# Kernel optimization log

Hardware: AMD Instinct MI355X
Metric: run time of the kernel (lower is better)

Reference implementation:

```python
import jax, jax.numpy as jnp
import numpy as np

N_NODES = 50000
N_EDGES = 800000
N_GRAPHS = 1024
BN_EPS = 1e-5

def _linear_params(key, fan_in, fan_out):
    k1, k2 = jax.random.split(key)
    lim = 1.0 / np.sqrt(fan_in)
    w = jax.random.uniform(k1, (fan_in, fan_out), jnp.float32, -lim, lim)
    b = jax.random.uniform(k2, (fan_out,), jnp.float32, -lim, lim)
    return w, b


def setup_inputs() -> dict:
    key = jax.random.key(0)
    ks = jax.random.split(key, 16)
    x = jax.random.normal(ks[0], (N_NODES, 114), jnp.float32)
    edge_index = jax.random.randint(ks[1], (2, N_EDGES), 0, N_NODES, jnp.int64)
    batch = jnp.sort(jax.random.randint(ks[2], (N_NODES,), 0, N_GRAPHS, jnp.int64))
    w1a, b1a = _linear_params(ks[3], 114, 198)
    w1b, b1b = _linear_params(ks[4], 198, 198)
    w2a, b2a = _linear_params(ks[5], 198, 64)
    w2b, b2b = _linear_params(ks[6], 64, 64)
    w3a, b3a = _linear_params(ks[7], 64, 32)
    w3b, b3b = _linear_params(ks[8], 32, 32)
    fw1, fb1 = _linear_params(ks[9], 32, 16)
    fw2, fb2 = _linear_params(ks[10], 16, 8)
    ow, ob = _linear_params(ks[11], 8, 2)
    g1 = jnp.ones((198,), jnp.float32); be1 = jnp.zeros((198,), jnp.float32)
    g2 = jnp.ones((64,), jnp.float32); be2 = jnp.zeros((64,), jnp.float32)
    g3 = jnp.ones((32,), jnp.float32); be3 = jnp.zeros((32,), jnp.float32)
    return dict(x=x, edge_index=edge_index, batch=batch,
                w1a=w1a, b1a=b1a, w1b=w1b, b1b=b1b, g1=g1, be1=be1,
                w2a=w2a, b2a=b2a, w2b=w2b, b2b=b2b, g2=g2, be2=be2,
                w3a=w3a, b3a=b3a, w3b=w3b, b3b=b3b, g3=g3, be3=be3,
                fw1=fw1, fb1=fb1, fw2=fw2, fb2=fb2, ow=ow, ob=ob)


def _gin_conv(x, src, dst, wa, ba, wb, bb):
    # GINConv, eps=0: h_i = MLP((1+eps)*x_i + sum_{j->i} x_j)
    agg = jax.ops.segment_sum(x[src], dst, num_segments=N_NODES)
    h = x + agg
    h = jax.nn.relu(h @ wa + ba) @ wb + bb
    return h


def _batchnorm(h, gamma, beta):
    # training-mode BN over the node axis (biased variance, as torch)
    mean = jnp.mean(h, axis=0)
    var = jnp.var(h, axis=0)
    return (h - mean) * jax.lax.rsqrt(var + BN_EPS) * gamma + beta


def reference(x, edge_index, batch,
              w1a, b1a, w1b, b1b, g1, be1,
              w2a, b2a, w2b, b2b, g2, be2,
              w3a, b3a, w3b, b3b, g3, be3,
              fw1, fb1, fw2, fb2, ow, ob):
    src, dst = edge_index[0], edge_index[1]
    h = jax.nn.relu(_gin_conv(x, src, dst, w1a, b1a, w1b, b1b))
    h = _batchnorm(h, g1, be1)
    h = jax.nn.relu(_gin_conv(h, src, dst, w2a, b2a, w2b, b2b))
    h = _batchnorm(h, g2, be2)
    h = jax.nn.relu(_gin_conv(h, src, dst, w3a, b3a, w3b, b3b))
    h = _batchnorm(h, g3, be3)
    g = jax.ops.segment_sum(h, batch, num_segments=N_GRAPHS)  # global_add_pool
    g = jax.nn.relu(g @ fw1 + fb1)
    g = jax.nn.relu(g @ fw2 + fb2)
    return g @ ow + ob
```

## Files before the change

kernel.cpp:

```cpp
#include <hip/hip_runtime.h>

#define NODES  50000
#define EDGES  800000
#define GRAPHS 1024
#define P      200

#define SCAN_BLK 256
#define SCAN_NB  ((NODES + SCAN_BLK - 1) / SCAN_BLK)

typedef __attribute__((ext_vector_type(8))) short short8v;
typedef __attribute__((ext_vector_type(4))) float f32x4;

__device__ __forceinline__ ushort f2bf(float f) {
    uint u = __float_as_uint(f);
    u = u + 0x7FFFu + ((u >> 16) & 1u);
    return (ushort)(u >> 16);
}

__global__ void hist_kernel(const int* __restrict__ dst, int* __restrict__ deg) {
    int e = blockIdx.x * blockDim.x + threadIdx.x;
    if (e < EDGES) atomicAdd(&deg[dst[e]], 1);
}

__global__ void scan_part(const int* __restrict__ deg, int* __restrict__ part) {
    __shared__ int sh[SCAN_BLK];
    int t = threadIdx.x;
    int n = blockIdx.x * SCAN_BLK + t;
    sh[t] = (n < NODES) ? deg[n] : 0;
    __syncthreads();
    for (int off = SCAN_BLK / 2; off > 0; off >>= 1) {
        if (t < off) sh[t] += sh[t + off];
        __syncthreads();
    }
    if (t == 0) part[blockIdx.x] = sh[0];
}

__global__ void scan_scan(int* __restrict__ part) {
    __shared__ int sh[SCAN_BLK];
    int t = threadIdx.x;
    int v = (t < SCAN_NB) ? part[t] : 0;
    sh[t] = v;
    __syncthreads();
    for (int off = 1; off < SCAN_BLK; off <<= 1) {
        int u = 0;
        if (t >= off) u = sh[t - off];
        __syncthreads();
        if (t >= off) sh[t] += u;
        __syncthreads();
    }
    if (t < SCAN_NB) part[t] = sh[t] - v;
}

__global__ void scan_expand(const int* __restrict__ deg, const int* __restrict__ part,
                            int* __restrict__ rowstart, int* __restrict__ cursor) {
    __shared__ int sh[SCAN_BLK];
    int t = threadIdx.x;
    int n = blockIdx.x * SCAN_BLK + t;
    int v = (n < NODES) ? deg[n] : 0;
    sh[t] = v;
    __syncthreads();
    for (int off = 1; off < SCAN_BLK; off <<= 1) {
        int u = 0;
        if (t >= off) u = sh[t - off];
        __syncthreads();
        if (t >= off) sh[t] += u;
        __syncthreads();
    }
    int excl = sh[t] - v + part[blockIdx.x];
    if (n < NODES) {
        rowstart[n] = excl;
        cursor[n]   = excl;
        if (n == NODES - 1) rowstart[NODES] = excl + v;
    }
}

__global__ void scatter_kernel(const int* __restrict__ src, const int* __restrict__ dst,
                               int* __restrict__ cursor, int* __restrict__ csrc) {
    int e = blockIdx.x * blockDim.x + threadIdx.x;
    if (e < EDGES) {
        int p = atomicAdd(&cursor[dst[e]], 1);
        csrc[p] = src[e];
    }
}

__global__ void pad_w_mfma(const float* __restrict__ W, int K, int N, int NCH, int CT,
                           ushort* __restrict__ out) {
    int s = blockIdx.x * blockDim.x + threadIdx.x;
    int half = NCH * CT * 512;
    if (s >= 2 * half) return;
    int h = s / half;
    int r = s % half;
    int j = r & 7, col = (r >> 3) & 15, kg = (r >> 7) & 3;
    int rest = r >> 9;
    int ct = rest % CT, c = rest / CT;
    int k = c * 32 + kg * 8 + j;
    int n = ct * 16 + col;
    float v = (k < K && n < N) ? W[k * N + n] : 0.0f;
    ushort hi = f2bf(v);
    if (h == 0) out[s] = hi;
    else {
        float hf = __uint_as_float(((uint)hi) << 16);
        out[s] = f2bf(v - hf);
    }
}

template<int D>
__global__ void csr_agg(const float* __restrict__ feat, int fpitch,
                        const int* __restrict__ rowstart, const int* __restrict__ csrc,
                        float* __restrict__ agg, int opitch) {
    int wid  = (blockIdx.x * blockDim.x + threadIdx.x) >> 6;
    int lane = threadIdx.x & 63;
    if (wid >= NODES) return;
    constexpr int NI  = (D + 63) / 64;
    constexpr int UNR = (NI == 1) ? 8 : 4;
    float s[NI];
#pragma unroll
    for (int i = 0; i < NI; i++) s[i] = 0.0f;
    const int r0 = rowstart[wid], r1 = rowstart[wid + 1];
    for (int base = r0; base < r1; base += 64) {
        const int myidx = (base + lane < r1) ? csrc[base + lane] : 0;
        const int cnt = min(64, r1 - base);
        int t = 0;
        for (; t + UNR <= cnt; t += UNR) {
            const float* p[UNR];
#pragma unroll
            for (int u = 0; u < UNR; u++)
                p[u] = feat + (size_t)__shfl(myidx, t + u) * fpitch;
            float v[UNR][NI];
#pragma unroll
            for (int u = 0; u < UNR; u++)
#pragma unroll
                for (int i = 0; i < NI; i++) {
                    int c = lane + 64 * i;
                    if (c < D) v[u][i] = p[u][c];
                }
#pragma unroll
            for (int i = 0; i < NI; i++) {
                int c = lane + 64 * i;
                if (c < D) {
                    float acc = 0.0f;
#pragma unroll
                    for (int u = 0; u < UNR; u++) acc += v[u][i];
                    s[i] += acc;
                }
            }
        }
        for (; t < cnt; t++) {
            const float* fp2 = feat + (size_t)__shfl(myidx, t) * fpitch;
#pragma unroll
            for (int i = 0; i < NI; i++) {
                int c = lane + 64 * i;
                if (c < D) s[i] += fp2[c];
            }
        }
    }
    float* ap = agg + (size_t)wid * opitch;
#pragma unroll
    for (int i = 0; i < NI; i++) {
        int c = lane + 64 * i;
        if (c < D) ap[c] = s[i];
    }
}

template<int K, int N, bool ADD2, bool STATS, bool BNX, bool PRE, bool ACT>
__launch_bounds__(256)
__global__ void gemm_mfma(const float* __restrict__ X, int xpitch,
                          const float* __restrict__ A2, int apitch,
                          const ushort* __restrict__ WF,
                          const float* __restrict__ B,
                          const float* __restrict__ PREB,
                          const float* __restrict__ scale, const float* __restrict__ shift,
                          float* __restrict__ OUT, int opitch,
                          float* __restrict__ gsum, float* __restrict__ gsq) {
    constexpr int KP  = ((K + 31) / 32) * 32;
    constexpr int NCH = KP / 32;
    constexpr int NP  = ((N + 63) / 64) * 64;
    constexpr int CT  = NP / 16;
    constexpr int CTW = CT / 4;
    static_assert(CT % 4 == 0, "col tiles must split across 4 waves");

    __shared__ __align__(16) ushort A_lds[2][4][4][16][8];
    __shared__ float shSum[STATS ? NP : 4];
    __shared__ float shSq [STATS ? NP : 4];

    const int tid  = threadIdx.x;
    const int lane = tid & 63;
    const int wv   = tid >> 6;
    const int node0 = blockIdx.x * 64;

    if (STATS) {
        for (int n = tid; n < NP; n += 256) { shSum[n] = 0.0f; shSq[n] = 0.0f; }
    }

    f32x4 acc[4][CTW] = {};

    const int sr  = tid >> 2;
    const int skg = tid & 3;
    const size_t fstride = (size_t)NCH * CT * 512;

    for (int c = 0; c < NCH; c++) {
        const int kbase = c * 32;
        {
            const int gn = node0 + sr;
            const int k0 = kbase + skg * 8;
            float v[8];
#pragma unroll
            for (int j = 0; j < 8; j++) {
                int gk = k0 + j;
                float t = 0.0f;
                if (gn < NODES && gk < K) {
                    t = X[(size_t)gn * xpitch + gk];
                    if (BNX) t = fmaf(t, scale[gk], shift[gk]);
                    if (ADD2) t += A2[(size_t)gn * apitch + gk];
                    if (PRE)  t = fmaxf(t + PREB[gk], 0.0f);
                }
                v[j] = t;
            }
            short8v hv, lv;
#pragma unroll
            for (int j = 0; j < 8; j++) {
                ushort h = f2bf(v[j]);
                float hf = __uint_as_float(((uint)h) << 16);
                ushort l = f2bf(v[j] - hf);
                hv[j] = (short)h; lv[j] = (short)l;
            }
            *(short8v*)&A_lds[0][sr >> 4][skg][sr & 15][0] = hv;
            *(short8v*)&A_lds[1][sr >> 4][skg][sr & 15][0] = lv;
        }
        __syncthreads();

        const int kg = lane >> 4, rw = lane & 15;
        short8v ah[4], al[4];
#pragma unroll
        for (int rt = 0; rt < 4; rt++) {
            ah[rt] = *(const short8v*)&A_lds[0][rt][kg][rw][0];
            al[rt] = *(const short8v*)&A_lds[1][rt][kg][rw][0];
        }
#pragma unroll
        for (int t = 0; t < CTW; t++) {
            const int ct = wv * CTW + t;
            const size_t fb = ((size_t)(c * CT + ct)) * 512 + (size_t)lane * 8;
            short8v wh = *(const short8v*)(WF + fb);
            short8v wl = *(const short8v*)(WF + fstride + fb);
#pragma unroll
            for (int rt = 0; rt < 4; rt++) {
                acc[rt][t] = __builtin_amdgcn_mfma_f32_16x16x32_bf16(ah[rt], wh, acc[rt][t], 0, 0, 0);
                acc[rt][t] = __builtin_amdgcn_mfma_f32_16x16x32_bf16(al[rt], wh, acc[rt][t], 0, 0, 0);
                acc[rt][t] = __builtin_amdgcn_mfma_f32_16x16x32_bf16(ah[rt], wl, acc[rt][t], 0, 0, 0);
            }
        }
        __syncthreads();
    }

    const int mg = lane >> 4, colb = lane & 15;
#pragma unroll
    for (int t = 0; t < CTW; t++) {
        const int ct = wv * CTW + t;
        const int n = ct * 16 + colb;
        const float bn = (ACT && n < N) ? B[n] : 0.0f;
        float psum = 0.0f, psq = 0.0f;
#pragma unroll
        for (int rt = 0; rt < 4; rt++) {
#pragma unroll
            for (int j = 0; j < 4; j++) {
                int m = node0 + rt * 16 + mg * 4 + j;
                float vv = ACT ? fmaxf(acc[rt][t][j] + bn, 0.0f) : acc[rt][t][j];
                if (m < NODES && n < N) {
                    OUT[(size_t)m * opitch + n] = vv;
                    if (STATS) { psum += vv; psq += vv * vv; }
                }
            }
        }
        if (STATS && n < N) {
            atomicAdd(&shSum[n], psum);
            atomicAdd(&shSq[n], psq);
        }
    }
    if (STATS) {
        __syncthreads();
        for (int n = tid; n < N; n += 256) {
            atomicAdd(&gsum[n], shSum[n]);
            atomicAdd(&gsq[n], shSq[n]);
        }
    }
}

template<int N>
__global__ void bn_finalize(const float* __restrict__ sum, const float* __restrict__ sq,
                            const float* __restrict__ gamma, const float* __restrict__ beta,
                            float* __restrict__ scale, float* __restrict__ shift) {
    int n = threadIdx.x;
    if (n < N) {
        float mean = sum[n] * (1.0f / NODES);
        float var  = sq[n] * (1.0f / NODES) - mean * mean;
        var = var < 0.0f ? 0.0f : var;
        float sc = gamma[n] * rsqrtf(var + 1e-5f);
        scale[n] = sc;
        shift[n] = beta[n] - mean * sc;
    }
}

__global__ void pool_kernel(const float* __restrict__ h, const int* __restrict__ batch,
                            const float* __restrict__ scale, const float* __restrict__ shift,
                            float* __restrict__ g) {
    int idx = blockIdx.x * blockDim.x + threadIdx.x;
    if (idx >= NODES * 32) return;
    int n = idx >> 5, f = idx & 31;
    float v = fmaf(h[(size_t)n * 32 + f], scale[f], shift[f]);
    atomicAdd(&g[batch[n] * 32 + f], v);
}

__global__ void head_kernel(const float* __restrict__ g,
                            const float* __restrict__ fw1, const float* __restrict__ fb1,
                            const float* __restrict__ fw2, const float* __restrict__ fb2,
                            const float* __restrict__ ow, const float* __restrict__ ob,
                            float* __restrict__ out) {
    int gi = blockIdx.x * blockDim.x + threadIdx.x;
    if (gi >= GRAPHS) return;
    float v[32];
#pragma unroll
    for (int k = 0; k < 32; k++) v[k] = g[gi * 32 + k];
    float a1[16];
#pragma unroll
    for (int o = 0; o < 16; o++) {
        float s = fb1[o];
#pragma unroll
        for (int k = 0; k < 32; k++) s = fmaf(v[k], fw1[k * 16 + o], s);
        a1[o] = s > 0.0f ? s : 0.0f;
    }
    float a2[8];
#pragma unroll
    for (int o = 0; o < 8; o++) {
        float s = fb2[o];
#pragma unroll
        for (int k = 0; k < 16; k++) s = fmaf(a1[k], fw2[k * 8 + o], s);
        a2[o] = s > 0.0f ? s : 0.0f;
    }
#pragma unroll
    for (int o = 0; o < 2; o++) {
        float s = ob[o];
#pragma unroll
        for (int k = 0; k < 8; k++) s = fmaf(a2[k], ow[k * 2 + o], s);
        out[gi * 2 + o] = s;
    }
}

extern "C" void kernel_launch(void* const* d_in, const int* in_sizes, int n_in,
                              void* d_out, int out_size, void* d_ws, size_t ws_size,
                              hipStream_t stream) {
    const float* x     = (const float*)d_in[0];
    const int*   ei    = (const int*)d_in[1];
    const int*   batch = (const int*)d_in[2];
    const float *w1a = (const float*)d_in[3],  *b1a = (const float*)d_in[4];
    const float *w1b = (const float*)d_in[5],  *b1b = (const float*)d_in[6];
    const float *g1  = (const float*)d_in[7],  *be1 = (const float*)d_in[8];
    const float *w2a = (const float*)d_in[9],  *b2a = (const float*)d_in[10];
    const float *w2b = (const float*)d_in[11], *b2b = (const float*)d_in[12];
    const float *g2  = (const float*)d_in[13], *be2 = (const float*)d_in[14];
    const float *w3a = (const float*)d_in[15], *b3a = (const float*)d_in[16];
    const float *w3b = (const float*)d_in[17], *b3b = (const float*)d_in[18];
    const float *g3  = (const float*)d_in[19], *be3 = (const float*)d_in[20];
    const float *fw1 = (const float*)d_in[21], *fb1 = (const float*)d_in[22];
    const float *fw2 = (const float*)d_in[23], *fb2 = (const float*)d_in[24];
    const float *ow  = (const float*)d_in[25], *ob  = (const float*)d_in[26];
    const int* src = ei;
    const int* dst = ei + EDGES;

    float* ws    = (float*)d_ws;
    float* b0    = ws;
    float* b1    = ws + (size_t)NODES * P;
    float* Y2    = b1;
    float* AG2   = b1 + (size_t)NODES * 64;
    float* Y3    = b1;
    float* AG3   = b1 + (size_t)NODES * 32;
    float* SUM   = ws + (size_t)2 * NODES * P;
    float* SQ    = SUM + 256;
    float* SCALE = SUM + 512;
    float* SHIFT = SUM + 768;
    float* G     = SUM + 1024;
    int*   deg      = (int*)(G + GRAPHS * 32);
    int*   rowstart = deg + NODES;
    int*   cursor   = rowstart + NODES + 1;
    int*   part     = cursor + NODES;
    int*   csrc     = part + 256;
    uintptr_t wfp = ((uintptr_t)(csrc + EDGES) + 15) & ~(uintptr_t)15;
    ushort* WF1 = (ushort*)wfp;
    ushort* WF2 = WF1 + 65536;
    ushort* WF3 = WF2 + 114688;
    ushort* WF4 = WF3 + 28672;
    ushort* WF5 = WF4 + 8192;
    ushort* WF6 = WF5 + 8192;
    float* out = (float*)d_out;

    const int GB64 = (NODES + 63) / 64;
    const int AB = (NODES * 64 + 255) / 256;
    const int EB = (EDGES + 255) / 256;

    pad_w_mfma<<<(65536 + 255) / 256, 256, 0, stream>>>(w1a, 114, 198, 4, 16, WF1);
    pad_w_mfma<<<(114688 + 255) / 256, 256, 0, stream>>>(w1b, 198, 198, 7, 16, WF2);
    pad_w_mfma<<<(28672 + 255) / 256, 256, 0, stream>>>(w2a, 198, 64, 7, 4, WF3);
    pad_w_mfma<<<(8192 + 255) / 256, 256, 0, stream>>>(w2b, 64, 64, 2, 4, WF4);
    pad_w_mfma<<<(8192 + 255) / 256, 256, 0, stream>>>(w3a, 64, 32, 2, 4, WF5);
    pad_w_mfma<<<(4096 + 255) / 256, 256, 0, stream>>>(w3b, 32, 32, 1, 4, WF6);

    hipMemsetAsync(deg, 0, NODES * sizeof(int), stream);
    hist_kernel<<<EB, 256, 0, stream>>>(dst, deg);
    scan_part<<<SCAN_NB, SCAN_BLK, 0, stream>>>(deg, part);
    scan_scan<<<1, SCAN_BLK, 0, stream>>>(part);
    scan_expand<<<SCAN_NB, SCAN_BLK, 0, stream>>>(deg, part, rowstart, cursor);
    scatter_kernel<<<EB, 256, 0, stream>>>(src, dst, cursor, csrc);

    csr_agg<114><<<AB, 256, 0, stream>>>(x, 114, rowstart, csrc, b0, P);
    gemm_mfma<114, 198, true, false, false, false, true><<<GB64, 256, 0, stream>>>(
        x, 114, b0, P, WF1, b1a, nullptr, nullptr, nullptr, b1, P, nullptr, nullptr);
    hipMemsetAsync(SUM, 0, 512 * sizeof(float), stream);
    gemm_mfma<198, 198, false, true, false, false, true><<<GB64, 256, 0, stream>>>(
        b1, P, nullptr, 0, WF2, b1b, nullptr, nullptr, nullptr, b0, P, SUM, SQ);
    bn_finalize<198><<<1, 256, 0, stream>>>(SUM, SQ, g1, be1, SCALE, SHIFT);

    gemm_mfma<198, 64, false, false, true, false, false><<<GB64, 256, 0, stream>>>(
        b0, P, nullptr, 0, WF3, nullptr, nullptr, SCALE, SHIFT, Y2, 64, nullptr, nullptr);
    csr_agg<64><<<AB, 256, 0, stream>>>(Y2, 64, rowstart, csrc, AG2, 64);
    hipMemsetAsync(SUM, 0, 512 * sizeof(float), stream);
    gemm_mfma<64, 64, true, true, false, true, true><<<GB64, 256, 0, stream>>>(
        Y2, 64, AG2, 64, WF4, b2b, b2a, nullptr, nullptr, b0, 64, SUM, SQ);
    bn_finalize<64><<<1, 256, 0, stream>>>(SUM, SQ, g2, be2, SCALE, SHIFT);

    gemm_mfma<64, 32, false, false, true, false, false><<<GB64, 256, 0, stream>>>(
        b0, 64, nullptr, 0, WF5, nullptr, nullptr, SCALE, SHIFT, Y3, 32, nullptr, nullptr);
    csr_agg<32><<<AB, 256, 0, stream>>>(Y3, 32, rowstart, csrc, AG3, 32);
    hipMemsetAsync(SUM, 0, 512 * sizeof(float), stream);
    gemm_mfma<32, 32, true, true, false, true, true><<<GB64, 256, 0, stream>>>(
        Y3, 32, AG3, 32, WF6, b3b, b3a, nullptr, nullptr, b0, 32, SUM, SQ);
    bn_finalize<32><<<1, 256, 0, stream>>>(SUM, SQ, g3, be3, SCALE, SHIFT);

    hipMemsetAsync(G, 0, GRAPHS * 32 * sizeof(float), stream);
    pool_kernel<<<(NODES * 32 + 255) / 256, 256, 0, stream>>>(b0, batch, SCALE, SHIFT, G);
    head_kernel<<<(GRAPHS + 255) / 256, 256, 0, stream>>>(G, fw1, fb1, fw2, fb2, ow, ob, out);
}
```

Before: 500.1 us.

## Double-buffer A tiles in LDS and prefetch weight fragments in MFMA GEMM

Splits the LDS A tile into two buffers so the global loads for the next K-chunk are issued before the current chunk's MFMAs, with conversion and storing done afterward. This removes one barrier per iteration. Weight fragments are register-prefetched one column tile ahead, and s_setprio raises wave priority around the MFMA bursts. The cost is more LDS and more registers held across the loop, which could reduce occupancy.

```diff
diff --git a/kernel.cpp b/kernel.cpp
--- a/kernel.cpp
+++ b/kernel.cpp
@@ -179,7 +179,7 @@
     constexpr int CTW = CT / 4;
     static_assert(CT % 4 == 0, "col tiles must split across 4 waves");
 
-    __shared__ __align__(16) ushort A_lds[2][4][4][16][8];
+    __shared__ __align__(16) ushort A_lds[2][2][4][4][16][8];
     __shared__ float shSum[STATS ? NP : 4];
     __shared__ float shSq [STATS ? NP : 4];
 
@@ -196,59 +196,83 @@
 
     const int sr  = tid >> 2;
     const int skg = tid & 3;
+    const int gn  = node0 + sr;
     const size_t fstride = (size_t)NCH * CT * 512;
 
+    float xv[8];
+    float a2v[ADD2 ? 8 : 1];
+
+    auto loadA = [&](int c) {
+        const int k0 = c * 32 + skg * 8;
+#pragma unroll
+        for (int j = 0; j < 8; j++) {
+            int gk = k0 + j;
+            bool ok = (gn < NODES && gk < K);
+            xv[j] = ok ? X[(size_t)gn * xpitch + gk] : 0.0f;
+            if (ADD2) a2v[j] = ok ? A2[(size_t)gn * apitch + gk] : 0.0f;
+        }
+    };
+    auto cvtStoreA = [&](int buf, int c) {
+        const int k0 = c * 32 + skg * 8;
+        short8v hv, lv;
+#pragma unroll
+        for (int j = 0; j < 8; j++) {
+            int gk = k0 + j;
+            float t = 0.0f;
+            if (gn < NODES && gk < K) {
+                t = xv[j];
+                if (BNX) t = fmaf(t, scale[gk], shift[gk]);
+                if (ADD2) t += a2v[j];
+                if (PRE)  t = fmaxf(t + PREB[gk], 0.0f);
+            }
+            ushort h = f2bf(t);
+            float hf = __uint_as_float(((uint)h) << 16);
+            ushort l = f2bf(t - hf);
+            hv[j] = (short)h; lv[j] = (short)l;
+        }
+        *(short8v*)&A_lds[buf][0][sr >> 4][skg][sr & 15][0] = hv;
+        *(short8v*)&A_lds[buf][1][sr >> 4][skg][sr & 15][0] = lv;
+    };
+
+    loadA(0);
+    cvtStoreA(0, 0);
+    __syncthreads();
+
+    const int kg = lane >> 4, rw = lane & 15;
     for (int c = 0; c < NCH; c++) {
-        const int kbase = c * 32;
-        {
-            const int gn = node0 + sr;
-            const int k0 = kbase + skg * 8;
-            float v[8];
-#pragma unroll
-            for (int j = 0; j < 8; j++) {
-                int gk = k0 + j;
-                float t = 0.0f;
-                if (gn < NODES && gk < K) {
-                    t = X[(size_t)gn * xpitch + gk];
-                    if (BNX) t = fmaf(t, scale[gk], shift[gk]);
-                    if (ADD2) t += A2[(size_t)gn * apitch + gk];
-                    if (PRE)  t = fmaxf(t + PREB[gk], 0.0f);
-                }
-                v[j] = t;
-            }
-            short8v hv, lv;
-#pragma unroll
-            for (int j = 0; j < 8; j++) {
-                ushort h = f2bf(v[j]);
-                float hf = __uint_as_float(((uint)h) << 16);
-                ushort l = f2bf(v[j] - hf);
-                hv[j] = (short)h; lv[j] = (short)l;
-            }
-            *(short8v*)&A_lds[0][sr >> 4][skg][sr & 15][0] = hv;
-            *(short8v*)&A_lds[1][sr >> 4][skg][sr & 15][0] = lv;
-        }
-        __syncthreads();
-
-        const int kg = lane >> 4, rw = lane & 15;
+        const int buf = c & 1;
+        if (c + 1 < NCH) loadA(c + 1);
+
         short8v ah[4], al[4];
 #pragma unroll
         for (int rt = 0; rt < 4; rt++) {
-            ah[rt] = *(const short8v*)&A_lds[0][rt][kg][rw][0];
-            al[rt] = *(const short8v*)&A_lds[1][rt][kg][rw][0];
-        }
+            ah[rt] = *(const short8v*)&A_lds[buf][0][rt][kg][rw][0];
+            al[rt] = *(const short8v*)&A_lds[buf][1][rt][kg][rw][0];
+        }
+
+        const size_t fb0 = ((size_t)(c * CT + wv * CTW)) * 512 + (size_t)lane * 8;
+        short8v wh = *(const short8v*)(WF + fb0);
+        short8v wl = *(const short8v*)(WF + fstride + fb0);
 #pragma unroll
         for (int t = 0; t < CTW; t++) {
-            const int ct = wv * CTW + t;
-            const size_t fb = ((size_t)(c * CT + ct)) * 512 + (size_t)lane * 8;
-            short8v wh = *(const short8v*)(WF + fb);
-            short8v wl = *(const short8v*)(WF + fstride + fb);
+            short8v nwh, nwl;
+            if (t + 1 < CTW) {
+                const size_t fb = fb0 + (size_t)(t + 1) * 512;
+                nwh = *(const short8v*)(WF + fb);
+                nwl = *(const short8v*)(WF + fstride + fb);
+            }
+            __builtin_amdgcn_s_setprio(1);
 #pragma unroll
             for (int rt = 0; rt < 4; rt++) {
                 acc[rt][t] = __builtin_amdgcn_mfma_f32_16x16x32_bf16(ah[rt], wh, acc[rt][t], 0, 0, 0);
                 acc[rt][t] = __builtin_amdgcn_mfma_f32_16x16x32_bf16(al[rt], wh, acc[rt][t], 0, 0, 0);
                 acc[rt][t] = __builtin_amdgcn_mfma_f32_16x16x32_bf16(ah[rt], wl, acc[rt][t], 0, 0, 0);
             }
-        }
+            __builtin_amdgcn_s_setprio(0);
+            if (t + 1 < CTW) { wh = nwh; wl = nwl; }
+        }
+
+        if (c + 1 < NCH) cvtStoreA((c + 1) & 1, c + 1);
         __syncthreads();
     }
 
```

Result: faster. 485.3 us (-3.0%).
